# Optimization experiments

Hardware: AMD Instinct MI355X
Metric: run time of the kernel (lower is better)

Reference implementation:

```python
import jax, jax.numpy as jnp
import numpy as np

EMBED = 256
HEADS = 8
HEAD_DIM = EMBED // HEADS  # 32
B, L = 2, 4096
END_X = END_Y = 64
THETA = 10000.0


def _axial_rope_tables(dim, end_x, end_y, theta):
    # dim = per-head dim (32); dim//4 = 8 freqs per axis -> 16 complex pairs
    freqs = 1.0 / theta ** (np.arange(0, dim, 4)[: dim // 4].astype(np.float32) / dim)
    t = np.arange(end_x * end_y, dtype=np.float32)
    t_x = t % end_x
    t_y = np.floor(t / end_x)
    ang_x = np.outer(t_x, freqs)  # [L, dim//4]
    ang_y = np.outer(t_y, freqs)
    ang = np.concatenate([ang_x, ang_y], axis=-1)  # [L, dim//2]
    return jnp.asarray(np.cos(ang)), jnp.asarray(np.sin(ang))

ROPE_COS, ROPE_SIN = _axial_rope_tables(HEAD_DIM, END_X, END_Y, THETA)


def _apply_rope(x, cos, sin):
    # x: [B, H, L, D]; interpret consecutive pairs as complex numbers
    b, h, l, d = x.shape
    xr = x.reshape(b, h, l, d // 2, 2)
    real, imag = xr[..., 0], xr[..., 1]
    c = cos[None, None, :, :]  # [1,1,L,D/2]
    s = sin[None, None, :, :]
    out_r = real * c - imag * s
    out_i = real * s + imag * c
    return jnp.stack([out_r, out_i], axis=-1).reshape(b, h, l, d)


def setup_inputs() -> dict:
    key = jax.random.key(0)
    ks = jax.random.split(key, 11)
    sw = 1.0 / np.sqrt(EMBED)
    inp = {
        'q': jax.random.normal(ks[0], (B, L, EMBED), jnp.float32),
        'k': jax.random.normal(ks[1], (B, L, EMBED), jnp.float32),
        'v': jax.random.normal(ks[2], (B, L, EMBED), jnp.float32),
        'Wq': jax.random.normal(ks[3], (EMBED, EMBED), jnp.float32) * sw,
        'bq': jnp.zeros((EMBED,), jnp.float32),
        'Wk': jax.random.normal(ks[4], (EMBED, EMBED), jnp.float32) * sw,
        'bk': jnp.zeros((EMBED,), jnp.float32),
        'Wv': jax.random.normal(ks[5], (EMBED, EMBED), jnp.float32) * sw,
        'bv': jnp.zeros((EMBED,), jnp.float32),
        'Wo': jax.random.normal(ks[6], (EMBED, EMBED), jnp.float32) * sw,
        'bo': jnp.zeros((EMBED,), jnp.float32),
    }
    return inp


def reference(q, k, v, Wq, bq, Wk, bk, Wv, bv, Wo, bo):
    b, l, _ = q.shape
    # QKV projections (torch Linear: x @ W.T + b)
    qp = q @ Wq.T + bq
    kp = k @ Wk.T + bk
    vp = v @ Wv.T + bv
    # separate heads -> [B, H, L, D]
    sep = lambda x: x.reshape(b, l, HEADS, HEAD_DIM).transpose(0, 2, 1, 3)
    qh, kh, vh = sep(qp), sep(kp), sep(vp)
    # rotary position encoding (fp32, complex pair multiply)
    qh = _apply_rope(qh, ROPE_COS, ROPE_SIN)
    kh = _apply_rope(kh, ROPE_COS, ROPE_SIN)
    # scaled dot-product attention
    scale = 1.0 / np.sqrt(HEAD_DIM)
    scores = jnp.einsum('bhqd,bhkd->bhqk', qh, kh) * scale
    attn = jax.nn.softmax(scores, axis=-1)
    out = jnp.einsum('bhqk,bhkd->bhqd', attn, vh)
    # recombine heads and output projection
    out = out.transpose(0, 2, 1, 3).reshape(b, l, EMBED)
    return out @ Wo.T + bo
```

## Files before the change

kernel.cpp:

```cpp
#include <hip/hip_runtime.h>

#define SEQ   4096
#define EMBED 256
#define HEADS 8
#define HDIM  32
#define BH    16
#define NROW  8192

typedef __bf16 bf16;
typedef bf16  bf16x8 __attribute__((ext_vector_type(8)));
typedef bf16  bf16x4 __attribute__((ext_vector_type(4)));
typedef float f32x4  __attribute__((ext_vector_type(4)));

static __device__ __forceinline__ bf16x4 cvt4(float4 v) {
  bf16x4 r;
  r.x = (bf16)v.x; r.y = (bf16)v.y; r.z = (bf16)v.z; r.w = (bf16)v.w;
  return r;
}

static __device__ __forceinline__ float fast_exp2(float x) {
  float r;
  asm volatile("v_exp_f32 %0, %1" : "=v"(r) : "v"(x));
  return r;
}

__global__ __launch_bounds__(256) void proj_kernel(
    const float* __restrict__ qx, const float* __restrict__ kx, const float* __restrict__ vx,
    const float* __restrict__ Wq, const float* __restrict__ bq,
    const float* __restrict__ Wk, const float* __restrict__ bk,
    const float* __restrict__ Wv, const float* __restrict__ bv,
    bf16* __restrict__ qh, bf16* __restrict__ kh, bf16* __restrict__ vt,
    float qscale)
{
  __shared__ alignas(16) bf16 As[64][72];
  __shared__ alignas(16) bf16 Bs[64][72];
  const int z = blockIdx.z;
  const float* X    = (z == 0) ? qx : (z == 1) ? kx : vx;
  const float* W    = (z == 0) ? Wq : (z == 1) ? Wk : Wv;
  const float* bias = (z == 0) ? bq : (z == 1) ? bk : bv;

  const int tid  = threadIdx.x;
  const int wave = tid >> 6;
  const int lane = tid & 63;
  const int quad = lane >> 4;
  const int l16  = lane & 15;
  const int row0 = blockIdx.x * 64;
  const int col0 = blockIdx.y * 64;

  f32x4 acc[4] = { {0.f,0.f,0.f,0.f},{0.f,0.f,0.f,0.f},
                   {0.f,0.f,0.f,0.f},{0.f,0.f,0.f,0.f} };

  for (int k0 = 0; k0 < EMBED; k0 += 64) {
#pragma unroll
    for (int p = 0; p < 4; ++p) {
      int f = p * 256 + tid;
      int r = f >> 4;
      int c = (f & 15) * 4;
      float4 av = *(const float4*)&X[(size_t)(row0 + r) * EMBED + k0 + c];
      *(bf16x4*)&As[r][c] = cvt4(av);
      float4 wv = *(const float4*)&W[(size_t)(col0 + r) * EMBED + k0 + c];
      *(bf16x4*)&Bs[r][c] = cvt4(wv);
    }
    __syncthreads();
#pragma unroll
    for (int kk = 0; kk < 2; ++kk) {
      bf16x8 a = *(const bf16x8*)&As[wave * 16 + l16][kk * 32 + quad * 8];
#pragma unroll
      for (int nt = 0; nt < 4; ++nt) {
        bf16x8 b = *(const bf16x8*)&Bs[nt * 16 + l16][kk * 32 + quad * 8];
        acc[nt] = __builtin_amdgcn_mfma_f32_16x16x32_bf16(a, b, acc[nt], 0, 0, 0);
      }
    }
    __syncthreads();
  }

  if (z < 2) {
    bf16* dst = z ? kh : qh;
    const float out_scale = z ? 1.0f : qscale;
#pragma unroll
    for (int nt = 0; nt < 4; ++nt) {
#pragma unroll
      for (int r = 0; r < 4; ++r) {
        int row = row0 + wave * 16 + quad * 4 + r;
        int col = col0 + nt * 16 + l16;
        float val = acc[nt][r] + bias[col];
        int l = row & (SEQ - 1);
        {
          float other = __shfl_xor(val, 1);
          int d = col & (HDIM - 1);
          int j = d >> 1;
          float fr = exp2f(-1.6609640474436813f * (float)(j & 7));
          float t  = (j < 8) ? (float)(l & 63) : (float)(l >> 6);
          float ang = t * fr;
          float sv, cv;
          sincosf(ang, &sv, &cv);
          val = (col & 1) ? (other * sv + val * cv) : (val * cv - other * sv);
        }
        val *= out_scale;
        int b = row >> 12;
        int h = col >> 5;
        int d = col & (HDIM - 1);
        dst[((size_t)((b * HEADS + h) * SEQ + l)) * HDIM + d] = (bf16)val;
      }
    }
  } else {
#pragma unroll
    for (int nt = 0; nt < 4; ++nt) {
      float bcol = bias[col0 + nt * 16 + l16];
      bf16x4 pk;
      pk.x = (bf16)(acc[nt][0] + bcol);
      pk.y = (bf16)(acc[nt][1] + bcol);
      pk.z = (bf16)(acc[nt][2] + bcol);
      pk.w = (bf16)(acc[nt][3] + bcol);
      *(bf16x4*)&As[nt * 16 + l16][wave * 16 + quad * 4] = pk;
    }
    __syncthreads();
    const int e   = tid >> 2;
    const int seg = tid & 3;
    const int ge  = col0 + e;
    const int hh  = ge >> 5;
    const int d   = ge & (HDIM - 1);
    const int bidx = row0 >> 12;
    const int l0   = row0 & (SEQ - 1);
    size_t dstbase = ((size_t)(bidx * HEADS + hh) * HDIM + d) * SEQ + l0 + seg * 16;
    bf16x8 t0 = *(const bf16x8*)&As[e][seg * 16];
    bf16x8 t1 = *(const bf16x8*)&As[e][seg * 16 + 8];
    *(bf16x8*)&vt[dstbase]     = t0;
    *(bf16x8*)&vt[dstbase + 8] = t1;
  }
}

__global__ __launch_bounds__(512, 4) void attn_kernel(
    const bf16* __restrict__ Q, const bf16* __restrict__ K,
    const bf16* __restrict__ Vt, bf16* __restrict__ H)
{
  __shared__ alignas(16) bf16 Ks[2][4][64][8];
  __shared__ alignas(16) bf16 Vs[2][4][64][8];
  __shared__ alignas(16) bf16 Pa[8][16][72];

  const int tid  = threadIdx.x;
  const int wave = tid >> 6;
  const int lane = tid & 63;
  const int quad = lane >> 4;
  const int l16  = lane & 15;

  const int id = blockIdx.x;
  const int bh = ((id & 7) << 1) | (id >> 8);
  const int q0 = ((id >> 3) & 31) * 128 + wave * 16;

  const bf16* Qg = Q  + (size_t)bh * SEQ * HDIM;
  const bf16* Kg = K  + (size_t)bh * SEQ * HDIM;
  const bf16* Vg = Vt + (size_t)bh * HDIM * SEQ;

  bf16x8 qf = *(const bf16x8*)&Qg[(size_t)(q0 + l16) * HDIM + quad * 8];

  f32x4 o0 = {0.f,0.f,0.f,0.f};
  f32x4 o1 = {0.f,0.f,0.f,0.f};
  float lsum = 0.f;

  const bool isK = tid < 256;
  const int  tt  = tid & 255;
  const bf16* sbase;
  size_t sstep;
  bf16* d0;
  if (isK) {
    const int r  = tt >> 2;
    const int qq = tt & 3;
    sbase = Kg + (size_t)r * HDIM + qq * 8;
    sstep = (size_t)64 * HDIM;
    d0 = &Ks[0][r >> 4][qq * 16 + (r & 15)][0];
  } else {
    const int d  = tt >> 3;
    const int sg = tt & 7;
    sbase = Vg + (size_t)d * SEQ + sg * 8;
    sstep = 64;
    d0 = &Vs[0][((d >> 4) << 1) | (sg >> 2)][(sg & 3) * 16 + (d & 15)][0];
  }
  bf16* d1 = d0 + 4 * 64 * 8;

  const f32x4 minit = {-12.f,-12.f,-12.f,-12.f};

  *(bf16x8*)d0 = *(const bf16x8*)sbase;
  __syncthreads();

  for (int t = 0; t < 64; ++t) {
    const int cur = t & 1;
    const int tn  = (t < 63) ? t + 1 : 63;
    bf16x8 g = *(const bf16x8*)&sbase[(size_t)tn * sstep];

    const bf16* KT = &Ks[cur][0][0][0];
    const bf16* VT = &Vs[cur][0][0][0];

    bf16x8 kf0 = *(const bf16x8*)&KT[(0 * 64 + lane) * 8];
    bf16x8 kf1 = *(const bf16x8*)&KT[(1 * 64 + lane) * 8];
    bf16x8 kf2 = *(const bf16x8*)&KT[(2 * 64 + lane) * 8];
    bf16x8 kf3 = *(const bf16x8*)&KT[(3 * 64 + lane) * 8];

    f32x4 s[4];
    s[0] = __builtin_amdgcn_mfma_f32_16x16x32_bf16(kf0, qf, minit, 0, 0, 0);
    s[1] = __builtin_amdgcn_mfma_f32_16x16x32_bf16(kf1, qf, minit, 0, 0, 0);
    s[2] = __builtin_amdgcn_mfma_f32_16x16x32_bf16(kf2, qf, minit, 0, 0, 0);
    s[3] = __builtin_amdgcn_mfma_f32_16x16x32_bf16(kf3, qf, minit, 0, 0, 0);

    bf16x8 vf0 = *(const bf16x8*)&VT[(0 * 64 + lane) * 8];
    bf16x8 vf1 = *(const bf16x8*)&VT[(1 * 64 + lane) * 8];
    bf16x8 vf2 = *(const bf16x8*)&VT[(2 * 64 + lane) * 8];
    bf16x8 vf3 = *(const bf16x8*)&VT[(3 * 64 + lane) * 8];

#pragma unroll
    for (int nt = 0; nt < 4; ++nt) {
      float p0 = fast_exp2(s[nt][0]);
      float p1 = fast_exp2(s[nt][1]);
      float p2 = fast_exp2(s[nt][2]);
      float p3 = fast_exp2(s[nt][3]);
      lsum += (p0 + p1) + (p2 + p3);
      bf16x4 pk;
      pk.x = (bf16)p0; pk.y = (bf16)p1; pk.z = (bf16)p2; pk.w = (bf16)p3;
      *(bf16x4*)&Pa[wave][l16][nt * 16 + quad * 4] = pk;
    }

    asm volatile("s_waitcnt lgkmcnt(0)" ::: "memory");

    bf16x8 pf0 = *(const bf16x8*)&Pa[wave][l16][quad * 8];
    bf16x8 pf1 = *(const bf16x8*)&Pa[wave][l16][32 + quad * 8];
    o0 = __builtin_amdgcn_mfma_f32_16x16x32_bf16(pf0, vf0, o0, 0, 0, 0);
    o0 = __builtin_amdgcn_mfma_f32_16x16x32_bf16(pf1, vf1, o0, 0, 0, 0);
    o1 = __builtin_amdgcn_mfma_f32_16x16x32_bf16(pf0, vf2, o1, 0, 0, 0);
    o1 = __builtin_amdgcn_mfma_f32_16x16x32_bf16(pf1, vf3, o1, 0, 0, 0);

    *(bf16x8*)(cur ? d0 : d1) = g;
    __syncthreads();
  }

  lsum += __shfl_xor(lsum, 16);
  lsum += __shfl_xor(lsum, 32);

  const int b = bh >> 3;
  const int h = bh & 7;
#pragma unroll
  for (int r = 0; r < 4; ++r) {
    float tot  = __shfl(lsum, quad * 4 + r);
    float invr = 1.0f / tot;
    int   qg   = q0 + quad * 4 + r;
    size_t base = ((size_t)(b * SEQ + qg)) * EMBED + h * HDIM;
    H[base + l16]      = (bf16)(o0[r] * invr);
    H[base + 16 + l16] = (bf16)(o1[r] * invr);
  }
}

__global__ __launch_bounds__(256) void out_proj_kernel(
    const bf16* __restrict__ Hm, const float* __restrict__ W,
    const float* __restrict__ bias, float* __restrict__ out)
{
  __shared__ alignas(16) bf16 As[64][72];
  __shared__ alignas(16) bf16 Bs[64][72];
  const int tid  = threadIdx.x;
  const int wave = tid >> 6;
  const int lane = tid & 63;
  const int quad = lane >> 4;
  const int l16  = lane & 15;
  const int row0 = blockIdx.x * 64;
  const int col0 = blockIdx.y * 64;

  f32x4 acc[4] = { {0.f,0.f,0.f,0.f},{0.f,0.f,0.f,0.f},
                   {0.f,0.f,0.f,0.f},{0.f,0.f,0.f,0.f} };

  for (int k0 = 0; k0 < EMBED; k0 += 64) {
#pragma unroll
    for (int p = 0; p < 2; ++p) {
      int f = p * 256 + tid;
      int r = f >> 3;
      int c = (f & 7) * 8;
      *(bf16x8*)&As[r][c] = *(const bf16x8*)&Hm[(size_t)(row0 + r) * EMBED + k0 + c];
    }
#pragma unroll
    for (int p = 0; p < 4; ++p) {
      int f = p * 256 + tid;
      int r = f >> 4;
      int c = (f & 15) * 4;
      float4 wv = *(const float4*)&W[(size_t)(col0 + r) * EMBED + k0 + c];
      *(bf16x4*)&Bs[r][c] = cvt4(wv);
    }
    __syncthreads();
#pragma unroll
    for (int kk = 0; kk < 2; ++kk) {
      bf16x8 a = *(const bf16x8*)&As[wave * 16 + l16][kk * 32 + quad * 8];
#pragma unroll
      for (int nt = 0; nt < 4; ++nt) {
        bf16x8 b = *(const bf16x8*)&Bs[nt * 16 + l16][kk * 32 + quad * 8];
        acc[nt] = __builtin_amdgcn_mfma_f32_16x16x32_bf16(a, b, acc[nt], 0, 0, 0);
      }
    }
    __syncthreads();
  }

#pragma unroll
  for (int nt = 0; nt < 4; ++nt) {
#pragma unroll
    for (int r = 0; r < 4; ++r) {
      int row = row0 + wave * 16 + quad * 4 + r;
      int col = col0 + nt * 16 + l16;
      out[(size_t)row * EMBED + col] = acc[nt][r] + bias[col];
    }
  }
}

extern "C" void kernel_launch(void* const* d_in, const int* in_sizes, int n_in,
                              void* d_out, int out_size, void* d_ws, size_t ws_size,
                              hipStream_t stream) {
  (void)in_sizes; (void)n_in; (void)out_size; (void)ws_size;
  const float* q  = (const float*)d_in[0];
  const float* k  = (const float*)d_in[1];
  const float* v  = (const float*)d_in[2];
  const float* Wq = (const float*)d_in[3];
  const float* bq = (const float*)d_in[4];
  const float* Wk = (const float*)d_in[5];
  const float* bk = (const float*)d_in[6];
  const float* Wv = (const float*)d_in[7];
  const float* bv = (const float*)d_in[8];
  const float* Wo = (const float*)d_in[9];
  const float* bo = (const float*)d_in[10];
  float* out = (float*)d_out;

  const size_t headElems = (size_t)BH * SEQ * HDIM;
  bf16* qh = (bf16*)d_ws;
  bf16* kh = qh + headElems;
  bf16* vt = kh + headElems;
  bf16* Hm = vt + headElems;

  const float qs = 0.2550436604f;

  proj_kernel<<<dim3(128, 4, 3), dim3(256), 0, stream>>>(q, k, v, Wq, bq, Wk, bk,
                                                         Wv, bv, qh, kh, vt, qs);
  attn_kernel<<<dim3(512), dim3(512), 0, stream>>>(qh, kh, vt, Hm);
  out_proj_kernel<<<dim3(128, 4), dim3(256), 0, stream>>>(Hm, Wo, bo, out);
}
```

Baseline: 173.3 us.

## Process two query tiles per wave in attention to reuse K/V fragments

After: 177.1 us. +2.1%, slower.

```diff
diff --git a/kernel.cpp b/kernel.cpp
--- a/kernel.cpp
+++ b/kernel.cpp
@@ -130,13 +130,14 @@
   }
 }
 
-__global__ __launch_bounds__(512, 4) void attn_kernel(
+__global__ __launch_bounds__(256, 4) void attn_kernel(
     const bf16* __restrict__ Q, const bf16* __restrict__ K,
     const bf16* __restrict__ Vt, bf16* __restrict__ H)
 {
   __shared__ alignas(16) bf16 Ks[2][4][64][8];
   __shared__ alignas(16) bf16 Vs[2][4][64][8];
-  __shared__ alignas(16) bf16 Pa[8][16][72];
+  __shared__ alignas(16) bf16 PaA[4][16][72];
+  __shared__ alignas(16) bf16 PaB[4][16][72];
 
   const int tid  = threadIdx.x;
   const int wave = tid >> 6;
@@ -146,47 +147,54 @@
 
   const int id = blockIdx.x;
   const int bh = ((id & 7) << 1) | (id >> 8);
-  const int q0 = ((id >> 3) & 31) * 128 + wave * 16;
+  const int q0 = ((id >> 3) & 31) * 128 + wave * 32;
 
   const bf16* Qg = Q  + (size_t)bh * SEQ * HDIM;
   const bf16* Kg = K  + (size_t)bh * SEQ * HDIM;
   const bf16* Vg = Vt + (size_t)bh * HDIM * SEQ;
 
-  bf16x8 qf = *(const bf16x8*)&Qg[(size_t)(q0 + l16) * HDIM + quad * 8];
-
-  f32x4 o0 = {0.f,0.f,0.f,0.f};
-  f32x4 o1 = {0.f,0.f,0.f,0.f};
-  float lsum = 0.f;
-
-  const bool isK = tid < 256;
-  const int  tt  = tid & 255;
+  bf16x8 qfA = *(const bf16x8*)&Qg[(size_t)(q0 +      l16) * HDIM + quad * 8];
+  bf16x8 qfB = *(const bf16x8*)&Qg[(size_t)(q0 + 16 + l16) * HDIM + quad * 8];
+
+  f32x4 oA0 = {0.f,0.f,0.f,0.f}, oA1 = {0.f,0.f,0.f,0.f};
+  f32x4 oB0 = {0.f,0.f,0.f,0.f}, oB1 = {0.f,0.f,0.f,0.f};
+  float lsumA = 0.f, lsumB = 0.f;
+
+  const bool isK = tid < 128;
+  const int  tt  = tid & 127;
   const bf16* sbase;
-  size_t sstep;
+  size_t sstep, soff2;
   bf16* d0;
   if (isK) {
     const int r  = tt >> 2;
     const int qq = tt & 3;
     sbase = Kg + (size_t)r * HDIM + qq * 8;
     sstep = (size_t)64 * HDIM;
+    soff2 = (size_t)32 * HDIM;
     d0 = &Ks[0][r >> 4][qq * 16 + (r & 15)][0];
   } else {
     const int d  = tt >> 3;
     const int sg = tt & 7;
     sbase = Vg + (size_t)d * SEQ + sg * 8;
     sstep = 64;
+    soff2 = (size_t)16 * SEQ;
     d0 = &Vs[0][((d >> 4) << 1) | (sg >> 2)][(sg & 3) * 16 + (d & 15)][0];
   }
-  bf16* d1 = d0 + 4 * 64 * 8;
+  bf16* d0b = d0 + 1024;
+  bf16* d1  = d0 + 2048;
+  bf16* d1b = d1 + 1024;
 
   const f32x4 minit = {-12.f,-12.f,-12.f,-12.f};
 
-  *(bf16x8*)d0 = *(const bf16x8*)sbase;
+  *(bf16x8*)d0  = *(const bf16x8*)sbase;
+  *(bf16x8*)d0b = *(const bf16x8*)&sbase[soff2];
   __syncthreads();
 
   for (int t = 0; t < 64; ++t) {
     const int cur = t & 1;
     const int tn  = (t < 63) ? t + 1 : 63;
-    bf16x8 g = *(const bf16x8*)&sbase[(size_t)tn * sstep];
+    bf16x8 g0 = *(const bf16x8*)&sbase[(size_t)tn * sstep];
+    bf16x8 g1 = *(const bf16x8*)&sbase[(size_t)tn * sstep + soff2];
 
     const bf16* KT = &Ks[cur][0][0][0];
     const bf16* VT = &Vs[cur][0][0][0];
@@ -196,11 +204,15 @@
     bf16x8 kf2 = *(const bf16x8*)&KT[(2 * 64 + lane) * 8];
     bf16x8 kf3 = *(const bf16x8*)&KT[(3 * 64 + lane) * 8];
 
-    f32x4 s[4];
-    s[0] = __builtin_amdgcn_mfma_f32_16x16x32_bf16(kf0, qf, minit, 0, 0, 0);
-    s[1] = __builtin_amdgcn_mfma_f32_16x16x32_bf16(kf1, qf, minit, 0, 0, 0);
-    s[2] = __builtin_amdgcn_mfma_f32_16x16x32_bf16(kf2, qf, minit, 0, 0, 0);
-    s[3] = __builtin_amdgcn_mfma_f32_16x16x32_bf16(kf3, qf, minit, 0, 0, 0);
+    f32x4 sA[4], sB[4];
+    sA[0] = __builtin_amdgcn_mfma_f32_16x16x32_bf16(kf0, qfA, minit, 0, 0, 0);
+    sA[1] = __builtin_amdgcn_mfma_f32_16x16x32_bf16(kf1, qfA, minit, 0, 0, 0);
+    sA[2] = __builtin_amdgcn_mfma_f32_16x16x32_bf16(kf2, qfA, minit, 0, 0, 0);
+    sA[3] = __builtin_amdgcn_mfma_f32_16x16x32_bf16(kf3, qfA, minit, 0, 0, 0);
+    sB[0] = __builtin_amdgcn_mfma_f32_16x16x32_bf16(kf0, qfB, minit, 0, 0, 0);
+    sB[1] = __builtin_amdgcn_mfma_f32_16x16x32_bf16(kf1, qfB, minit, 0, 0, 0);
+    sB[2] = __builtin_amdgcn_mfma_f32_16x16x32_bf16(kf2, qfB, minit, 0, 0, 0);
+    sB[3] = __builtin_amdgcn_mfma_f32_16x16x32_bf16(kf3, qfB, minit, 0, 0, 0);
 
     bf16x8 vf0 = *(const bf16x8*)&VT[(0 * 64 + lane) * 8];
     bf16x8 vf1 = *(const bf16x8*)&VT[(1 * 64 + lane) * 8];
@@ -209,42 +221,69 @@
 
 #pragma unroll
     for (int nt = 0; nt < 4; ++nt) {
-      float p0 = fast_exp2(s[nt][0]);
-      float p1 = fast_exp2(s[nt][1]);
-      float p2 = fast_exp2(s[nt][2]);
-      float p3 = fast_exp2(s[nt][3]);
-      lsum += (p0 + p1) + (p2 + p3);
+      float p0 = fast_exp2(sA[nt][0]);
+      float p1 = fast_exp2(sA[nt][1]);
+      float p2 = fast_exp2(sA[nt][2]);
+      float p3 = fast_exp2(sA[nt][3]);
+      lsumA += (p0 + p1) + (p2 + p3);
       bf16x4 pk;
       pk.x = (bf16)p0; pk.y = (bf16)p1; pk.z = (bf16)p2; pk.w = (bf16)p3;
-      *(bf16x4*)&Pa[wave][l16][nt * 16 + quad * 4] = pk;
+      *(bf16x4*)&PaA[wave][l16][nt * 16 + quad * 4] = pk;
+    }
+#pragma unroll
+    for (int nt = 0; nt < 4; ++nt) {
+      float p0 = fast_exp2(sB[nt][0]);
+      float p1 = fast_exp2(sB[nt][1]);
+      float p2 = fast_exp2(sB[nt][2]);
+      float p3 = fast_exp2(sB[nt][3]);
+      lsumB += (p0 + p1) + (p2 + p3);
+      bf16x4 pk;
+      pk.x = (bf16)p0; pk.y = (bf16)p1; pk.z = (bf16)p2; pk.w = (bf16)p3;
+      *(bf16x4*)&PaB[wave][l16][nt * 16 + quad * 4] = pk;
     }
 
     asm volatile("s_waitcnt lgkmcnt(0)" ::: "memory");
 
-    bf16x8 pf0 = *(const bf16x8*)&Pa[wave][l16][quad * 8];
-    bf16x8 pf1 = *(const bf16x8*)&Pa[wave][l16][32 + quad * 8];
-    o0 = __builtin_amdgcn_mfma_f32_16x16x32_bf16(pf0, vf0, o0, 0, 0, 0);
-    o0 = __builtin_amdgcn_mfma_f32_16x16x32_bf16(pf1, vf1, o0, 0, 0, 0);
-    o1 = __builtin_amdgcn_mfma_f32_16x16x32_bf16(pf0, vf2, o1, 0, 0, 0);
-    o1 = __builtin_amdgcn_mfma_f32_16x16x32_bf16(pf1, vf3, o1, 0, 0, 0);
-
-    *(bf16x8*)(cur ? d0 : d1) = g;
-    __syncthreads();
-  }
-
-  lsum += __shfl_xor(lsum, 16);
-  lsum += __shfl_xor(lsum, 32);
+    bf16x8 pfA0 = *(const bf16x8*)&PaA[wave][l16][quad * 8];
+    bf16x8 pfA1 = *(const bf16x8*)&PaA[wave][l16][32 + quad * 8];
+    bf16x8 pfB0 = *(const bf16x8*)&PaB[wave][l16][quad * 8];
+    bf16x8 pfB1 = *(const bf16x8*)&PaB[wave][l16][32 + quad * 8];
+    oA0 = __builtin_amdgcn_mfma_f32_16x16x32_bf16(pfA0, vf0, oA0, 0, 0, 0);
+    oA0 = __builtin_amdgcn_mfma_f32_16x16x32_bf16(pfA1, vf1, oA0, 0, 0, 0);
+    oA1 = __builtin_amdgcn_mfma_f32_16x16x32_bf16(pfA0, vf2, oA1, 0, 0, 0);
+    oA1 = __builtin_amdgcn_mfma_f32_16x16x32_bf16(pfA1, vf3, oA1, 0, 0, 0);
+    oB0 = __builtin_amdgcn_mfma_f32_16x16x32_bf16(pfB0, vf0, oB0, 0, 0, 0);
+    oB0 = __builtin_amdgcn_mfma_f32_16x16x32_bf16(pfB1, vf1, oB0, 0, 0, 0);
+    oB1 = __builtin_amdgcn_mfma_f32_16x16x32_bf16(pfB0, vf2, oB1, 0, 0, 0);
+    oB1 = __builtin_amdgcn_mfma_f32_16x16x32_bf16(pfB1, vf3, oB1, 0, 0, 0);
+
+    *(bf16x8*)(cur ? d0  : d1 ) = g0;
+    *(bf16x8*)(cur ? d0b : d1b) = g1;
+    __syncthreads();
+  }
+
+  lsumA += __shfl_xor(lsumA, 16);
+  lsumA += __shfl_xor(lsumA, 32);
+  lsumB += __shfl_xor(lsumB, 16);
+  lsumB += __shfl_xor(lsumB, 32);
 
   const int b = bh >> 3;
   const int h = bh & 7;
 #pragma unroll
   for (int r = 0; r < 4; ++r) {
-    float tot  = __shfl(lsum, quad * 4 + r);
-    float invr = 1.0f / tot;
-    int   qg   = q0 + quad * 4 + r;
-    size_t base = ((size_t)(b * SEQ + qg)) * EMBED + h * HDIM;
-    H[base + l16]      = (bf16)(o0[r] * invr);
-    H[base + 16 + l16] = (bf16)(o1[r] * invr);
+    float totA  = __shfl(lsumA, quad * 4 + r);
+    float invA  = 1.0f / totA;
+    int   qgA   = q0 + quad * 4 + r;
+    size_t baseA = ((size_t)(b * SEQ + qgA)) * EMBED + h * HDIM;
+    H[baseA + l16]      = (bf16)(oA0[r] * invA);
+    H[baseA + 16 + l16] = (bf16)(oA1[r] * invA);
+
+    float totB  = __shfl(lsumB, quad * 4 + r);
+    float invB  = 1.0f / totB;
+    int   qgB   = q0 + 16 + quad * 4 + r;
+    size_t baseB = ((size_t)(b * SEQ + qgB)) * EMBED + h * HDIM;
+    H[baseB + l16]      = (bf16)(oB0[r] * invB);
+    H[baseB + 16 + l16] = (bf16)(oB1[r] * invB);
   }
 }
 
@@ -332,6 +371,6 @@
 
   proj_kernel<<<dim3(128, 4, 3), dim3(256), 0, stream>>>(q, k, v, Wq, bq, Wk, bk,
                                                          Wv, bv, qh, kh, vt, qs);
-  attn_kernel<<<dim3(512), dim3(512), 0, stream>>>(qh, kh, vt, Hm);
+  attn_kernel<<<dim3(512), dim3(256), 0, stream>>>(qh, kh, vt, Hm);
   out_proj_kernel<<<dim3(128, 4), dim3(256), 0, stream>>>(Hm, Wo, bo, out);
 }
```
